# Kernel optimization log

Measured on AMD Instinct MI355X. Metric: run time of the kernel, lower is better.

Reference implementation:

```python
import jax, jax.numpy as jnp
import numpy as np

N_NODES = 100000
N_EDGES = 1200000
IN_CH = 64
HID_CH = 64
OUT_CH = 64
N_REL = 5
N_CLS = 8


def setup_inputs() -> dict:
    key = jax.random.key(0)
    ks = jax.random.split(key, 12)
    x = jax.random.normal(ks[0], (N_NODES, IN_CH), dtype=jnp.float32)
    edge_index = jax.random.randint(ks[1], (2, N_EDGES), 0, N_NODES, dtype=jnp.int64)
    edge_type = jax.random.randint(ks[2], (N_EDGES,), 0, N_REL, dtype=jnp.int64)
    s1 = 1.0 / np.sqrt(IN_CH)
    s2 = 1.0 / np.sqrt(HID_CH)
    s3 = 1.0 / np.sqrt(OUT_CH)
    W1 = jax.random.uniform(ks[3], (N_REL, IN_CH, HID_CH), jnp.float32, -s1, s1)
    root1 = jax.random.uniform(ks[4], (IN_CH, HID_CH), jnp.float32, -s1, s1)
    b1 = jax.random.uniform(ks[5], (HID_CH,), jnp.float32, -s1, s1)
    W2 = jax.random.uniform(ks[6], (N_REL, HID_CH, OUT_CH), jnp.float32, -s2, s2)
    root2 = jax.random.uniform(ks[7], (HID_CH, OUT_CH), jnp.float32, -s2, s2)
    b2 = jax.random.uniform(ks[8], (OUT_CH,), jnp.float32, -s2, s2)
    Wc = jax.random.uniform(ks[9], (OUT_CH, N_CLS), jnp.float32, -s3, s3)
    bc = jax.random.uniform(ks[10], (N_CLS,), jnp.float32, -s3, s3)
    return {"x": x, "edge_index": edge_index, "edge_type": edge_type,
            "W1": W1, "root1": root1, "b1": b1,
            "W2": W2, "root2": root2, "b2": b2,
            "Wc": Wc, "bc": bc}


def _rgcn_conv(x, src, dst, edge_type, W, root, bias):
    # PyG RGCNConv (no bases, aggr='mean', root_weight=True, bias=True):
    # out[i] = x[i] @ root + bias + sum_r mean_{(j->i) in rel r} x[j] @ W[r]
    n = x.shape[0]
    out = x @ root + bias
    xs = x[src]  # [E, d] gather once, reused across relations
    for r in range(N_REL):
        w = (edge_type == r).astype(x.dtype)  # [E]
        msg_sum = jax.ops.segment_sum(xs * w[:, None], dst, num_segments=n)  # [N, d]
        cnt = jax.ops.segment_sum(w, dst, num_segments=n)                    # [N]
        agg = msg_sum / jnp.maximum(cnt, 1.0)[:, None]
        out = out + agg @ W[r]
    return out


def reference(x, edge_index, edge_type, W1, root1, b1, W2, root2, b2, Wc, bc):
    src, dst = edge_index[0], edge_index[1]
    h = _rgcn_conv(x, src, dst, edge_type, W1, root1, b1)
    h = jax.nn.relu(h)
    h = _rgcn_conv(h, src, dst, edge_type, W2, root2, b2)
    logits = h @ Wc + bc
    return (h, logits)
```

## Files before the change

### kernel.cpp

```cpp
#include <hip/hip_runtime.h>

#define NN 100000
#define NE 1200000
#define CH 64
#define NREL 5
#define NCLS 8
#define SLOT 64
#define KTOT 384
#define HPAD 66

typedef _Float16 f16;
typedef _Float16 f16x2 __attribute__((ext_vector_type(2)));
typedef _Float16 f16x4 __attribute__((ext_vector_type(4)));
typedef _Float16 f16x8 __attribute__((ext_vector_type(8)));
typedef float f32x4 __attribute__((ext_vector_type(4)));

#define RFL __builtin_amdgcn_readfirstlane

__global__ __launch_bounds__(256) void cvt_f16_kernel(const float* __restrict__ x,
                                                      f16* __restrict__ xh) {
    int t = blockIdx.x * 256 + threadIdx.x;
    if (t >= NN * CH / 4) return;
    float4 v = reinterpret_cast<const float4*>(x)[t];
    f16x4 h = {(f16)v.x, (f16)v.y, (f16)v.z, (f16)v.w};
    *reinterpret_cast<f16x4*>(xh + (size_t)t * 4) = h;
}

__global__ __launch_bounds__(256) void scatter_kernel(const int* __restrict__ src,
                                                      const int* __restrict__ dst,
                                                      const int* __restrict__ et,
                                                      int* __restrict__ cursor,
                                                      int* __restrict__ sorted) {
    int e = blockIdx.x * 256 + threadIdx.x;
    if (e >= NE) return;
    int d = dst[e];
    int pos = atomicAdd(&cursor[d], 1);
    if (pos < SLOT) sorted[(size_t)d * SLOT + pos] = src[e] | (et[e] << 17);
}

__global__ __launch_bounds__(256, 8) void sort_rel(const int* __restrict__ cursor,
                                                   int* __restrict__ sorted) {
    int wv = threadIdx.x >> 6;
    int node = blockIdx.x * 4 + RFL(wv);
    if (node >= NN) return;
    int lane = threadIdx.x & 63;
    int deg = cursor[node];
    if (deg > SLOT) deg = SLOT;
    int w = sorted[(size_t)node * SLOT + lane];
    uint r = (uint)w >> 17;
    bool valid = lane < deg;
    unsigned long long b0 = __ballot(valid && r == 0);
    unsigned long long b1 = __ballot(valid && r == 1);
    unsigned long long b2 = __ballot(valid && r == 2);
    unsigned long long b3 = __ballot(valid && r == 3);
    unsigned long long b4 = __ballot(valid && r == 4);
    int st1 = (int)__popcll(b0);
    int st2 = st1 + (int)__popcll(b1);
    int st3 = st2 + (int)__popcll(b2);
    int st4 = st3 + (int)__popcll(b3);
    unsigned long long below = (1ull << lane) - 1ull;
    unsigned long long br = (r == 0) ? b0 : (r == 1) ? b1 : (r == 2) ? b2 : (r == 3) ? b3 : b4;
    int str = (r == 0) ? 0 : (r == 1) ? st1 : (r == 2) ? st2 : (r == 3) ? st3 : st4;
    int pos = str + (int)__popcll(br & below);
    if (valid) sorted[(size_t)node * SLOT + pos] = w;
}

__global__ __launch_bounds__(256) void prep_weights(const float* __restrict__ root1,
                                                    const float* __restrict__ W1,
                                                    const float* __restrict__ root2,
                                                    const float* __restrict__ W2,
                                                    f16* __restrict__ Btg) {
    int o = blockIdx.x * 256 + threadIdx.x;
    if (o >= 2 * 64 * KTOT) return;
    int layer = o / (64 * KTOT);
    int rem = o % (64 * KTOT);
    int n = rem / KTOT, k = rem % KTOT;
    const float* R = layer ? root2 : root1;
    const float* W = layer ? W2 : W1;
    float v = (k < CH) ? R[k * CH + n] : W[(size_t)(k - CH) * CH + n];
    Btg[o] = (f16)v;
}

template<bool CLS>
__global__ __launch_bounds__(256, 8) void fused_layer2(
    const f16* __restrict__ in, const f16* __restrict__ Btg,
    const float* __restrict__ bias,
    const int* __restrict__ cursor, const int* __restrict__ sorted,
    float* __restrict__ outf, f16* __restrict__ outh,
    const float* __restrict__ Wc, const float* __restrict__ bc,
    float* __restrict__ logits) {
    __shared__ __align__(16) char smem[16 * 784];
    f16* Ap = (f16*)smem;

    const int tid = threadIdx.x;
    const int wv = tid >> 6, lane = tid & 63;
    const int wvu = RFL(wv);
    const int ch2 = lane & 31;
    const bool lo32 = lane < 32;
    const int nb0 = blockIdx.x * 16;
    const f16x2 hz2 = {(f16)0.f, (f16)0.f};

#define LADP(RS, HV, INC)                                              \
    if ((RS) == 0)      { A0 += (HV); c0 += (INC); }                   \
    else if ((RS) == 1) { A1 += (HV); c1 += (INC); }                   \
    else if ((RS) == 2) { A2 += (HV); c2 += (INC); }                   \
    else if ((RS) == 3) { A3 += (HV); c3 += (INC); }                   \
    else                { A4 += (HV); c4 += (INC); }

#define PAIR(WA, WB, E0) {                                             \
    int w0 = RFL(WA);                                                  \
    int w1 = RFL(WB);                                                  \
    bool full = ((E0) + 1 < deg);                                      \
    if (!full) w1 = w0;                                                \
    uint r0 = (uint)w0 >> 17, r1 = (uint)w1 >> 17;                     \
    uint b0a = ((uint)w0 & 0x1FFFF) * 128u + (uint)ch2 * 4u;           \
    uint b1a = ((uint)w1 & 0x1FFFF) * 128u + (uint)ch2 * 4u;           \
    uint off = lo32 ? b0a : b1a;                                       \
    uint vv = *(const uint*)((const char*)in + off);                   \
    if (!full) vv = lo32 ? vv : 0u;                                    \
    f16x2 hv = __builtin_bit_cast(f16x2, vv);                          \
    if (r0 == r1) { int inc = full ? 2 : 1; LADP(r0, hv, inc) }        \
    else {                                                             \
        f16x2 hva = lo32 ? hv : hz2;                                   \
        f16x2 hvb = lo32 ? hz2 : hv;                                   \
        LADP(r0, hva, 1)                                               \
        LADP(r1, hvb, 1)                                               \
    }                                                                  \
}

#define MST(AV, SC, M) {                                               \
    int _ai = __builtin_bit_cast(int, AV);                             \
    int _bi = __shfl_xor(_ai, 32);                                     \
    f16x2 _t = AV + __builtin_bit_cast(f16x2, _bi);                    \
    if (lo32) {                                                        \
        f16x2 _o = {(f16)((float)_t.x * (SC)), (f16)((float)_t.y * (SC))}; \
        *(uint*)((char*)arow + (M) * 128 + ch2 * 4) = __builtin_bit_cast(uint, _o); \
    }                                                                  \
}

    for (int q = 0; q < 4; ++q) {
        int nl = wvu * 4 + q;
        int i = nb0 + nl;
        f16* arow = Ap + nl * 392;
        if (i >= NN) {
#pragma unroll
            for (int m = 0; m < 6; ++m) arow[m * 64 + lane] = (f16)0.f;
            continue;
        }
        int deg = cursor[i];
        if (deg > SLOT) deg = SLOT;
        const int* sp = sorted + (size_t)i * SLOT;

        f16 sv = in[(size_t)i * CH + lane];
        f16x2 A0 = hz2, A1 = hz2, A2 = hz2, A3 = hz2, A4 = hz2;
        int c0 = 0, c1 = 0, c2 = 0, c3 = 0, c4 = 0;

        if (deg > 0) {
            int npairs = (deg + 1) >> 1;
            int4 pk = *(const int4*)sp;
            for (int p0 = 0; p0 < npairs; p0 += 2) {
                int4 nx = *(const int4*)(sp + 2 * p0 + 4);
                PAIR(pk.x, pk.y, 2 * p0)
                if (p0 + 1 < npairs) PAIR(pk.z, pk.w, 2 * p0 + 2)
                pk = nx;
            }
        }

        arow[lane] = sv;
        float s0 = 1.0f / (float)(c0 > 0 ? c0 : 1);
        float s1 = 1.0f / (float)(c1 > 0 ? c1 : 1);
        float s2 = 1.0f / (float)(c2 > 0 ? c2 : 1);
        float s3 = 1.0f / (float)(c3 > 0 ? c3 : 1);
        float s4 = 1.0f / (float)(c4 > 0 ? c4 : 1);
        MST(A0, s0, 1) MST(A1, s1, 2) MST(A2, s2, 3) MST(A3, s3, 4) MST(A4, s4, 5)
    }
#undef PAIR
#undef LADP
#undef MST
    __syncthreads();

    const int col = lane & 15, lg = lane >> 4;
    float bv = bias[wvu * 16 + col];
    f32x4 acc = {bv, bv, bv, bv};
    const char* Ab = (const char*)Ap + col * 784 + lg * 16;
    const char* Bb = (const char*)Btg + (size_t)(wvu * 16 + col) * 768 + lg * 16;
#pragma unroll
    for (int k = 0; k < KTOT / 32; ++k) {
        f16x8 af = *(const f16x8*)(Ab + k * 64);
        f16x8 bf = *(const f16x8*)(Bb + k * 64);
        acc = __builtin_amdgcn_mfma_f32_16x16x32_f16(af, bf, acc, 0, 0, 0);
    }

    if (!CLS) {
#pragma unroll
        for (int r = 0; r < 4; ++r) {
            int node = nb0 + lg * 4 + r;
            if (node < NN)
                outh[(size_t)node * CH + wvu * 16 + col] = (f16)fmaxf(acc[r], 0.f);
        }
    } else {
        __syncthreads();
        float* hst = (float*)smem;
#pragma unroll
        for (int r = 0; r < 4; ++r) {
            int nl = lg * 4 + r;
            int node = nb0 + nl;
            hst[nl * HPAD + wvu * 16 + col] = acc[r];
            if (node < NN)
                outf[(size_t)node * CH + wvu * 16 + col] = acc[r];
        }
        __syncthreads();
        float wcr[NCLS];
#pragma unroll
        for (int c = 0; c < NCLS; ++c) wcr[c] = Wc[lane * NCLS + c];
        for (int q = 0; q < 4; ++q) {
            int nl = wvu * 4 + q;
            int i = nb0 + nl;
            if (i >= NN) continue;
            float v = hst[nl * HPAD + lane];
            float p[NCLS];
#pragma unroll
            for (int c = 0; c < NCLS; ++c) p[c] = v * wcr[c];
#pragma unroll
            for (int off = 32; off > 0; off >>= 1) {
#pragma unroll
                for (int c = 0; c < NCLS; ++c) p[c] += __shfl_xor(p[c], off);
            }
            if (lane == 0) {
                float4 lo = make_float4(p[0] + bc[0], p[1] + bc[1], p[2] + bc[2], p[3] + bc[3]);
                float4 hi = make_float4(p[4] + bc[4], p[5] + bc[5], p[6] + bc[6], p[7] + bc[7]);
                *reinterpret_cast<float4*>(&logits[(size_t)i * NCLS]) = lo;
                *reinterpret_cast<float4*>(&logits[(size_t)i * NCLS + 4]) = hi;
            }
        }
    }
}

extern "C" void kernel_launch(void* const* d_in, const int* in_sizes, int n_in,
                              void* d_out, int out_size, void* d_ws, size_t ws_size,
                              hipStream_t stream) {
    const float* x     = (const float*)d_in[0];
    const int*   ei    = (const int*)d_in[1];
    const int*   et    = (const int*)d_in[2];
    const float* W1    = (const float*)d_in[3];
    const float* root1 = (const float*)d_in[4];
    const float* b1    = (const float*)d_in[5];
    const float* W2    = (const float*)d_in[6];
    const float* root2 = (const float*)d_in[7];
    const float* b2    = (const float*)d_in[8];
    const float* Wc    = (const float*)d_in[9];
    const float* bc    = (const float*)d_in[10];
    const int* src = ei;
    const int* dst = ei + NE;

    float* h2     = (float*)d_out;
    float* logits = h2 + (size_t)NN * CH;

    int* cursor = (int*)d_ws;
    int* sorted = cursor + NN;
    f16* h1h    = (f16*)(sorted + (size_t)NN * SLOT + 16);
    f16* xh     = h1h + (size_t)NN * CH;
    f16* Btg    = xh + (size_t)NN * CH;

    (void)hipMemsetAsync(cursor, 0, (size_t)NN * 4, stream);
    cvt_f16_kernel<<<(NN * CH / 4 + 255) / 256, 256, 0, stream>>>(x, xh);
    scatter_kernel<<<(NE + 255) / 256, 256, 0, stream>>>(src, dst, et, cursor, sorted);
    sort_rel<<<(NN + 3) / 4, 256, 0, stream>>>(cursor, sorted);
    prep_weights<<<(2 * 64 * KTOT + 255) / 256, 256, 0, stream>>>(root1, W1, root2, W2, Btg);

    int nBlk = (NN + 15) / 16;
    fused_layer2<false><<<nBlk, 256, 0, stream>>>(
        xh, Btg, b1, cursor, sorted, nullptr, h1h, nullptr, nullptr, nullptr);
    fused_layer2<true><<<nBlk, 256, 0, stream>>>(
        h1h, Btg + (size_t)64 * KTOT, b2, cursor, sorted, h2, nullptr, Wc, bc, logits);
}
```

Before: 331.7 us.

## Merge convert and scatter kernels, unroll gather to four edge pairs in flight

Combines the fp32-to-fp16 conversion and the edge scatter into a single launch that splits its blocks between the two jobs, which removes one kernel launch and lets the two memory-bound jobs run at the same time. In the fused layer kernel, the neighbour gather loop now handles four edge pairs per iteration: all four gather loads are issued before any accumulation, so more memory requests are in flight at once. Source indices are clamped to stay in range, because the unrolled loop can read stale slots past the node's degree. The cost is higher register pressure and more prefetching of the sorted-edge array.

```diff
diff --git a/kernel.cpp b/kernel.cpp
--- a/kernel.cpp
+++ b/kernel.cpp
@@ -17,25 +17,24 @@
 
 #define RFL __builtin_amdgcn_readfirstlane
 
-__global__ __launch_bounds__(256) void cvt_f16_kernel(const float* __restrict__ x,
-                                                      f16* __restrict__ xh) {
-    int t = blockIdx.x * 256 + threadIdx.x;
-    if (t >= NN * CH / 4) return;
-    float4 v = reinterpret_cast<const float4*>(x)[t];
-    f16x4 h = {(f16)v.x, (f16)v.y, (f16)v.z, (f16)v.w};
-    *reinterpret_cast<f16x4*>(xh + (size_t)t * 4) = h;
-}
-
-__global__ __launch_bounds__(256) void scatter_kernel(const int* __restrict__ src,
-                                                      const int* __restrict__ dst,
-                                                      const int* __restrict__ et,
-                                                      int* __restrict__ cursor,
-                                                      int* __restrict__ sorted) {
-    int e = blockIdx.x * 256 + threadIdx.x;
-    if (e >= NE) return;
-    int d = dst[e];
-    int pos = atomicAdd(&cursor[d], 1);
-    if (pos < SLOT) sorted[(size_t)d * SLOT + pos] = src[e] | (et[e] << 17);
+__global__ __launch_bounds__(256) void cvt_scatter_kernel(
+    const float* __restrict__ x, f16* __restrict__ xh,
+    const int* __restrict__ src, const int* __restrict__ dst,
+    const int* __restrict__ et, int* __restrict__ cursor,
+    int* __restrict__ sorted, int cvtB) {
+    if ((int)blockIdx.x < cvtB) {
+        int t = blockIdx.x * 256 + threadIdx.x;
+        if (t >= NN * CH / 4) return;
+        float4 v = reinterpret_cast<const float4*>(x)[t];
+        f16x4 h = {(f16)v.x, (f16)v.y, (f16)v.z, (f16)v.w};
+        *reinterpret_cast<f16x4*>(xh + (size_t)t * 4) = h;
+    } else {
+        int e = (blockIdx.x - cvtB) * 256 + threadIdx.x;
+        if (e >= NE) return;
+        int d = dst[e];
+        int pos = atomicAdd(&cursor[d], 1);
+        if (pos < SLOT) sorted[(size_t)d * SLOT + pos] = src[e] | (et[e] << 17);
+    }
 }
 
 __global__ __launch_bounds__(256, 8) void sort_rel(const int* __restrict__ cursor,
@@ -97,8 +96,11 @@
     const int wvu = RFL(wv);
     const int ch2 = lane & 31;
     const bool lo32 = lane < 32;
+    const uint choff = (uint)ch2 * 4u;
     const int nb0 = blockIdx.x * 16;
     const f16x2 hz2 = {(f16)0.f, (f16)0.f};
+
+#define SBASE(W) ({ uint _s = (uint)(W) & 0x1FFFFu; _s = _s < (uint)NN ? _s : 0u; _s * 128u; })
 
 #define LADP(RS, HV, INC)                                              \
     if ((RS) == 0)      { A0 += (HV); c0 += (INC); }                   \
@@ -107,24 +109,17 @@
     else if ((RS) == 3) { A3 += (HV); c3 += (INC); }                   \
     else                { A4 += (HV); c4 += (INC); }
 
-#define PAIR(WA, WB, E0) {                                             \
-    int w0 = RFL(WA);                                                  \
-    int w1 = RFL(WB);                                                  \
-    bool full = ((E0) + 1 < deg);                                      \
-    if (!full) w1 = w0;                                                \
-    uint r0 = (uint)w0 >> 17, r1 = (uint)w1 >> 17;                     \
-    uint b0a = ((uint)w0 & 0x1FFFF) * 128u + (uint)ch2 * 4u;           \
-    uint b1a = ((uint)w1 & 0x1FFFF) * 128u + (uint)ch2 * 4u;           \
-    uint off = lo32 ? b0a : b1a;                                       \
-    uint vv = *(const uint*)((const char*)in + off);                   \
-    if (!full) vv = lo32 ? vv : 0u;                                    \
-    f16x2 hv = __builtin_bit_cast(f16x2, vv);                          \
-    if (r0 == r1) { int inc = full ? 2 : 1; LADP(r0, hv, inc) }        \
+#define PACC(WA, WB, FULL, VV) {                                       \
+    uint _r0 = (uint)(WA) >> 17, _r1 = (uint)(WB) >> 17;               \
+    uint _v = (VV);                                                    \
+    if (!(FULL)) _v = lo32 ? _v : 0u;                                  \
+    f16x2 _hv = __builtin_bit_cast(f16x2, _v);                         \
+    if (_r0 == _r1) { int _inc = (FULL) ? 2 : 1; LADP(_r0, _hv, _inc) }\
     else {                                                             \
-        f16x2 hva = lo32 ? hv : hz2;                                   \
-        f16x2 hvb = lo32 ? hz2 : hv;                                   \
-        LADP(r0, hva, 1)                                               \
-        LADP(r1, hvb, 1)                                               \
+        f16x2 _ha = lo32 ? _hv : hz2;                                  \
+        f16x2 _hb = lo32 ? hz2 : _hv;                                  \
+        LADP(_r0, _ha, 1)                                              \
+        LADP(_r1, _hb, 1)                                              \
     }                                                                  \
 }
 
@@ -157,12 +152,36 @@
 
         if (deg > 0) {
             int npairs = (deg + 1) >> 1;
-            int4 pk = *(const int4*)sp;
-            for (int p0 = 0; p0 < npairs; p0 += 2) {
-                int4 nx = *(const int4*)(sp + 2 * p0 + 4);
-                PAIR(pk.x, pk.y, 2 * p0)
-                if (p0 + 1 < npairs) PAIR(pk.z, pk.w, 2 * p0 + 2)
-                pk = nx;
+            int4 pk  = *(const int4*)sp;
+            int4 pk2 = *(const int4*)(sp + 4);
+            for (int p0 = 0; p0 < npairs; p0 += 4) {
+                int4 nx  = *(const int4*)(sp + 2 * p0 + 8);
+                int4 nx2 = *(const int4*)(sp + 2 * p0 + 12);
+                int w0a = RFL(pk.x),  w0b = RFL(pk.y);
+                int w1a = RFL(pk.z),  w1b = RFL(pk.w);
+                int w2a = RFL(pk2.x), w2b = RFL(pk2.y);
+                int w3a = RFL(pk2.z), w3b = RFL(pk2.w);
+                bool f0 = 2 * p0 + 1 < deg;
+                bool v1 = p0 + 1 < npairs, f1 = 2 * p0 + 3 < deg;
+                bool v2 = p0 + 2 < npairs, f2 = 2 * p0 + 5 < deg;
+                bool v3 = p0 + 3 < npairs, f3 = 2 * p0 + 7 < deg;
+                if (!f0) w0b = w0a;
+                if (!f1) w1b = w1a;
+                if (!f2) w2b = w2a;
+                if (!f3) w3b = w3a;
+                uint off0 = (lo32 ? SBASE(w0a) : SBASE(w0b)) + choff;
+                uint off1 = (lo32 ? SBASE(w1a) : SBASE(w1b)) + choff;
+                uint off2 = (lo32 ? SBASE(w2a) : SBASE(w2b)) + choff;
+                uint off3 = (lo32 ? SBASE(w3a) : SBASE(w3b)) + choff;
+                uint vv0 = *(const uint*)((const char*)in + off0);
+                uint vv1 = *(const uint*)((const char*)in + off1);
+                uint vv2 = *(const uint*)((const char*)in + off2);
+                uint vv3 = *(const uint*)((const char*)in + off3);
+                PACC(w0a, w0b, f0, vv0)
+                if (v1) PACC(w1a, w1b, f1, vv1)
+                if (v2) PACC(w2a, w2b, f2, vv2)
+                if (v3) PACC(w3a, w3b, f3, vv3)
+                pk = nx; pk2 = nx2;
             }
         }
 
@@ -174,9 +193,10 @@
         float s4 = 1.0f / (float)(c4 > 0 ? c4 : 1);
         MST(A0, s0, 1) MST(A1, s1, 2) MST(A2, s2, 3) MST(A3, s3, 4) MST(A4, s4, 5)
     }
-#undef PAIR
+#undef PACC
 #undef LADP
 #undef MST
+#undef SBASE
     __syncthreads();
 
     const int col = lane & 15, lg = lane >> 4;
@@ -263,8 +283,9 @@
     f16* Btg    = xh + (size_t)NN * CH;
 
     (void)hipMemsetAsync(cursor, 0, (size_t)NN * 4, stream);
-    cvt_f16_kernel<<<(NN * CH / 4 + 255) / 256, 256, 0, stream>>>(x, xh);
-    scatter_kernel<<<(NE + 255) / 256, 256, 0, stream>>>(src, dst, et, cursor, sorted);
+    int cvtB = (NN * CH / 4 + 255) / 256;
+    int sctB = (NE + 255) / 256;
+    cvt_scatter_kernel<<<cvtB + sctB, 256, 0, stream>>>(x, xh, src, dst, et, cursor, sorted, cvtB);
     sort_rel<<<(NN + 3) / 4, 256, 0, stream>>>(cursor, sorted);
     prep_weights<<<(2 * 64 * KTOT + 255) / 256, 256, 0, stream>>>(root1, W1, root2, W2, Btg);
 
```

Result: faster. 304.2 us (-8.3%).
